# Kernel optimization log

Hardware: AMD Instinct MI355X
Metric: run time of the kernel (lower is better)

## Reference

```python
import jax, jax.numpy as jnp
import numpy as np

N, E, F_IN, C, ED = 10000, 40000, 128, 32, 4000
NEG_SLOPE = 0.2


def setup_inputs() -> dict:
    key = jax.random.key(0)
    ks = jax.random.split(key, 16)
    s = 0.05
    return {
        "x": jax.random.normal(ks[0], (N, F_IN), jnp.float32),
        "edge_index": jax.random.randint(ks[1], (2, E), 0, N, dtype=jnp.int64),
        "edge_attr": jax.random.normal(ks[2], (E, ED), jnp.float32),
        # layer 1 params
        "W1": jax.random.normal(ks[3], (F_IN, C), jnp.float32) * s,
        "a_src1": jax.random.normal(ks[4], (C,), jnp.float32) * s,
        "a_dst1": jax.random.normal(ks[5], (C,), jnp.float32) * s,
        "We1": jax.random.normal(ks[6], (ED, C), jnp.float32) * s,
        "a_e1": jax.random.normal(ks[7], (C,), jnp.float32) * s,
        "b1": jnp.zeros((C,), jnp.float32),
        # layer 2 params
        "W2": jax.random.normal(ks[8], (C, C), jnp.float32) * s,
        "a_src2": jax.random.normal(ks[9], (C,), jnp.float32) * s,
        "a_dst2": jax.random.normal(ks[10], (C,), jnp.float32) * s,
        "We2": jax.random.normal(ks[11], (ED, C), jnp.float32) * s,
        "a_e2": jax.random.normal(ks[12], (C,), jnp.float32) * s,
        "b2": jnp.zeros((C,), jnp.float32),
    }


def gat_layer(x, src, dst, edge_attr, W, a_src, a_dst, We, a_e, b):
    # node transform (shared src/dst linear, heads=1)
    h = x @ W                                   # [N, C]
    # project edge features first (lin_edge has no bias, so this commutes
    # with the 'mean' fill of self-loop edge_attr)
    e_proj = edge_attr @ We                     # [E, C]
    # self-loop edge features = scatter-mean of projected edge_attr by dst
    cnt = jax.ops.segment_sum(jnp.ones((src.shape[0],), h.dtype), dst, N)
    loop_e = jax.ops.segment_sum(e_proj, dst, N) / jnp.maximum(cnt, 1.0)[:, None]
    # append self loops -> E_full = E + N (static)
    ar = jnp.arange(N, dtype=src.dtype)
    src_f = jnp.concatenate([src, ar])
    dst_f = jnp.concatenate([dst, ar])
    e_full = jnp.concatenate([e_proj, loop_e], axis=0)   # [E+N, C]
    # attention logits
    alpha = (h @ a_src)[src_f] + (h @ a_dst)[dst_f] + e_full @ a_e
    alpha = jax.nn.leaky_relu(alpha, NEG_SLOPE)
    # segment softmax over incoming edges of each destination node
    m = jax.ops.segment_max(alpha, dst_f, N)
    alpha = jnp.exp(alpha - m[dst_f])
    denom = jax.ops.segment_sum(alpha, dst_f, N)
    alpha = alpha / (denom[dst_f] + 1e-16)
    # weighted scatter-add aggregation
    out = jax.ops.segment_sum(h[src_f] * alpha[:, None], dst_f, N)
    return out + b


def reference(x, edge_index, edge_attr,
              W1, a_src1, a_dst1, We1, a_e1, b1,
              W2, a_src2, a_dst2, We2, a_e2, b2):
    src, dst = edge_index[0], edge_index[1]
    z = gat_layer(x, src, dst, edge_attr, W1, a_src1, a_dst1, We1, a_e1, b1)
    z = jax.nn.relu(z)
    z = gat_layer(z, src, dst, edge_attr, W2, a_src2, a_dst2, We2, a_e2, b2)
    return z
```

## Files before the change

kernel.cpp:

```cpp
#include <hip/hip_runtime.h>

#define NN   10000
#define EE   40000
#define FIN  128
#define CC   32
#define EDIM 4000

#define OFF_CNT      0
#define OFF_EA1      10240
#define OFF_EA2      50240
#define OFF_SEA1     90240
#define OFF_SEA2     100480
#define OFF_DEN1     110720
#define OFF_DEN2     120960
#define OFF_AGG1     131200
#define OFF_AGG2     451200
#define ZERO_FLOATS  771200
#define OFF_SRC      771200
#define OFF_DST      812160
#define OFF_H1       853120
#define OFF_HS1      1173120
#define OFF_HD1      1183360
#define OFF_P1       1193600
#define OFF_PL1      1234560
#define OFF_Z1       1244800
#define OFF_H2       1564800
#define OFF_HS2      1884800
#define OFF_HD2      1895040
#define OFF_P2       1905280
#define OFF_PL2      1946240

__global__ __launch_bounds__(256) void detect_convert(
    const void* __restrict__ ei, int* __restrict__ srcI, int* __restrict__ dstI,
    int* __restrict__ cnt)
{
    const int* w = (const int*)ei;
    bool is64 = ((w[1] | w[3] | w[5] | w[7] | w[9] | w[11] | w[13] | w[15]) == 0);
    int i = blockIdx.x * 256 + threadIdx.x;
    if (i < EE) {
        int s, d;
        if (is64) {
            const long long* e64 = (const long long*)ei;
            s = (int)e64[i];
            d = (int)e64[EE + i];
        } else {
            s = w[i];
            d = w[EE + i];
        }
        srcI[i] = s;
        dstI[i] = d;
        atomicAdd(&cnt[d], 1);
    }
}

__global__ __launch_bounds__(256) void edge_gemm(
    const float* __restrict__ EA,
    const float* __restrict__ We1, const float* __restrict__ We2,
    const float* __restrict__ ae1, const float* __restrict__ ae2,
    float* __restrict__ ea1g, float* __restrict__ ea2g)
{
    __shared__ __align__(16) float As[64][68];
    __shared__ __align__(16) float Bs[64][68];

    const int t    = threadIdx.x;
    const int row0 = blockIdx.x * 64;
    const int c0   = blockIdx.y * 16;
    const int c1   = min(c0 + 16, 63);

    const int tm = t >> 4, tn = t & 15;
    const int lrow = t >> 2, ls = t & 3;

    float acc[4][4] = {};

    const float* Arow = EA + (size_t)(row0 + lrow) * EDIM;

    for (int ch = c0; ch < c1; ++ch) {
        const int k0 = ch * 64;
        #pragma unroll
        for (int j = 0; j < 4; ++j) {
            int kk = 4 * (ls + 4 * j);
            int kg = k0 + kk;
            float4 v = make_float4(0.f, 0.f, 0.f, 0.f);
            if (kg < EDIM) v = *(const float4*)(Arow + kg);
            As[kk + 0][lrow] = v.x;
            As[kk + 1][lrow] = v.y;
            As[kk + 2][lrow] = v.z;
            As[kk + 3][lrow] = v.w;
        }
        {
            int kg = k0 + lrow;
            #pragma unroll
            for (int j = 0; j < 4; ++j) {
                int col4 = 4 * (ls + 4 * j);
                float4 v = make_float4(0.f, 0.f, 0.f, 0.f);
                if (kg < EDIM) {
                    const float* src = (col4 < 32)
                        ? (We1 + (size_t)kg * 32 + col4)
                        : (We2 + (size_t)kg * 32 + (col4 - 32));
                    v = *(const float4*)src;
                }
                *(float4*)&Bs[lrow][col4] = v;
            }
        }
        __syncthreads();
        #pragma unroll 4
        for (int kk = 0; kk < 64; ++kk) {
            float4 a4 = *(float4*)&As[kk][tm << 2];
            float4 b4 = *(float4*)&Bs[kk][tn << 2];
            float av[4] = {a4.x, a4.y, a4.z, a4.w};
            float bv[4] = {b4.x, b4.y, b4.z, b4.w};
            #pragma unroll
            for (int i = 0; i < 4; ++i)
                #pragma unroll
                for (int j = 0; j < 4; ++j)
                    acc[i][j] += av[i] * bv[j];
        }
        __syncthreads();
    }

    float* red = &As[0][0];
    if (t < 128) red[t] = 0.f;
    __syncthreads();
    const int half = tn >> 3;
    const int colL = (tn << 2) - (half << 5);
    const float* ae = half ? ae2 : ae1;
    const float a0 = ae[colL], a1 = ae[colL + 1], a2 = ae[colL + 2], a3 = ae[colL + 3];
    #pragma unroll
    for (int i = 0; i < 4; ++i) {
        float sP = acc[i][0] * a0 + acc[i][1] * a1 + acc[i][2] * a2 + acc[i][3] * a3;
        atomicAdd(&red[(((tm << 2) + i) << 1) + half], sP);
    }
    __syncthreads();
    if (t < 128) {
        int row = t >> 1, hh = t & 1;
        float* dstp = hh ? ea2g : ea1g;
        atomicAdd(&dstp[row0 + row], red[t]);
    }
}

__global__ __launch_bounds__(256) void scatter_sum_ea(
    const int* __restrict__ dstI,
    const float* __restrict__ ea1, const float* __restrict__ ea2,
    float* __restrict__ se1, float* __restrict__ se2)
{
    int i = blockIdx.x * 256 + threadIdx.x;
    if (i < EE) {
        int d = dstI[i];
        atomicAdd(&se1[d], ea1[i]);
        atomicAdd(&se2[d], ea2[i]);
    }
}

template <int K>
__global__ __launch_bounds__(256) void node_transform(
    const float* __restrict__ X, const float* __restrict__ Wg,
    const float* __restrict__ a_src, const float* __restrict__ a_dst,
    float* __restrict__ h, float* __restrict__ hs, float* __restrict__ hd)
{
    __shared__ __align__(16) float Wl[K * 32];
    __shared__ __align__(16) float Xl[64][K];
    __shared__ float Hl[64][33];

    const int t = threadIdx.x;
    const int row0 = blockIdx.x * 64;

    for (int idx = t; idx < K * 8; idx += 256)
        ((float4*)Wl)[idx] = ((const float4*)Wg)[idx];
    for (int idx = t; idx < 64 * (K / 4); idx += 256) {
        int r = idx / (K / 4), kq = idx % (K / 4);
        int gr = row0 + r;
        float4 v = make_float4(0.f, 0.f, 0.f, 0.f);
        if (gr < NN) v = ((const float4*)(X + (size_t)gr * K))[kq];
        *(float4*)&Xl[r][kq * 4] = v;
    }
    __syncthreads();

    const int c = t & 31, rb = t >> 5;
    #pragma unroll
    for (int j = 0; j < 8; ++j) {
        int r = rb * 8 + j;
        float accv = 0.f;
        for (int k = 0; k < K; ++k) accv += Xl[r][k] * Wl[k * 32 + c];
        Hl[r][c] = accv;
        int gr = row0 + r;
        if (gr < NN) h[(size_t)gr * 32 + c] = accv;
    }
    __syncthreads();

    if (t < 64) {
        int gr = row0 + t;
        if (gr < NN) {
            float s1 = 0.f, s2 = 0.f;
            #pragma unroll
            for (int cc = 0; cc < 32; ++cc) {
                float hv = Hl[t][cc];
                s1 += hv * a_src[cc];
                s2 += hv * a_dst[cc];
            }
            hs[gr] = s1;
            hd[gr] = s2;
        }
    }
}

__global__ __launch_bounds__(256) void edge_softmax(
    const int* __restrict__ srcI, const int* __restrict__ dstI,
    const float* __restrict__ hs, const float* __restrict__ hd,
    const float* __restrict__ ea, const float* __restrict__ sum_ea,
    const int* __restrict__ cnt,
    float* __restrict__ pe, float* __restrict__ ploop, float* __restrict__ denom)
{
    int i = blockIdx.x * 256 + threadIdx.x;
    if (i < EE) {
        int s = srcI[i], d = dstI[i];
        float a = hs[s] + hd[d] + ea[i];
        a = a > 0.f ? a : 0.2f * a;
        float p = expf(a);
        pe[i] = p;
        atomicAdd(&denom[d], p);
    } else if (i < EE + NN) {
        int n = i - EE;
        float cf = (float)cnt[n];
        cf = cf < 1.f ? 1.f : cf;
        float a = hs[n] + hd[n] + sum_ea[n] / cf;
        a = a > 0.f ? a : 0.2f * a;
        float p = expf(a);
        ploop[n] = p;
        atomicAdd(&denom[n], p);
    }
}

__global__ __launch_bounds__(256) void aggregate(
    const int* __restrict__ srcI, const int* __restrict__ dstI,
    const float* __restrict__ h, const float* __restrict__ pe,
    const float* __restrict__ ploop, float* __restrict__ agg)
{
    int gid = blockIdx.x * 256 + threadIdx.x;
    int i = gid >> 3;
    int c4 = (gid & 7) << 2;
    if (i >= EE + NN) return;
    int s, d;
    float p;
    if (i < EE) {
        s = srcI[i]; d = dstI[i]; p = pe[i];
    } else {
        s = d = i - EE; p = ploop[s];
    }
    const float4 hv = *(const float4*)&h[(size_t)s * 32 + c4];
    float* ag = &agg[(size_t)d * 32 + c4];
    atomicAdd(ag + 0, p * hv.x);
    atomicAdd(ag + 1, p * hv.y);
    atomicAdd(ag + 2, p * hv.z);
    atomicAdd(ag + 3, p * hv.w);
}

__global__ __launch_bounds__(256) void finalize(
    const float* __restrict__ agg, const float* __restrict__ denom,
    const float* __restrict__ bias, float* __restrict__ out, int relu)
{
    int gid = blockIdx.x * 256 + threadIdx.x;
    if (gid >= NN * 32) return;
    int n = gid >> 5, cidx = gid & 31;
    float v = agg[gid] / (denom[n] + 1e-16f) + bias[cidx];
    if (relu) v = v > 0.f ? v : 0.f;
    out[gid] = v;
}

extern "C" void kernel_launch(void* const* d_in, const int* in_sizes, int n_in,
                              void* d_out, int out_size, void* d_ws, size_t ws_size,
                              hipStream_t stream)
{
    const float* x    = (const float*)d_in[0];
    const void*  ei   = d_in[1];
    const float* eatt = (const float*)d_in[2];
    const float* W1   = (const float*)d_in[3];
    const float* as1  = (const float*)d_in[4];
    const float* ad1  = (const float*)d_in[5];
    const float* We1  = (const float*)d_in[6];
    const float* ae1  = (const float*)d_in[7];
    const float* b1   = (const float*)d_in[8];
    const float* W2   = (const float*)d_in[9];
    const float* as2  = (const float*)d_in[10];
    const float* ad2  = (const float*)d_in[11];
    const float* We2  = (const float*)d_in[12];
    const float* ae2  = (const float*)d_in[13];
    const float* b2   = (const float*)d_in[14];
    float* out = (float*)d_out;
    float* w   = (float*)d_ws;

    hipMemsetAsync(d_ws, 0, (size_t)ZERO_FLOATS * 4, stream);

    int*   cnt  = (int*)(w + OFF_CNT);
    float* ea1v = w + OFF_EA1;
    float* ea2v = w + OFF_EA2;
    float* sea1 = w + OFF_SEA1;
    float* sea2 = w + OFF_SEA2;
    float* den1 = w + OFF_DEN1;
    float* den2 = w + OFF_DEN2;
    float* agg1 = w + OFF_AGG1;
    float* agg2 = w + OFF_AGG2;
    int*   srcI = (int*)(w + OFF_SRC);
    int*   dstI = (int*)(w + OFF_DST);
    float* h1   = w + OFF_H1;
    float* hs1  = w + OFF_HS1;
    float* hd1  = w + OFF_HD1;
    float* p1   = w + OFF_P1;
    float* pl1  = w + OFF_PL1;
    float* z1   = w + OFF_Z1;
    float* h2   = w + OFF_H2;
    float* hs2  = w + OFF_HS2;
    float* hd2  = w + OFF_HD2;
    float* p2   = w + OFF_P2;
    float* pl2  = w + OFF_PL2;

    detect_convert<<<157, 256, 0, stream>>>(ei, srcI, dstI, cnt);

    edge_gemm<<<dim3(625, 4), 256, 0, stream>>>(eatt, We1, We2, ae1, ae2, ea1v, ea2v);
    scatter_sum_ea<<<157, 256, 0, stream>>>(dstI, ea1v, ea2v, sea1, sea2);

    node_transform<128><<<157, 256, 0, stream>>>(x, W1, as1, ad1, h1, hs1, hd1);
    edge_softmax<<<196, 256, 0, stream>>>(srcI, dstI, hs1, hd1, ea1v, sea1, cnt, p1, pl1, den1);
    aggregate<<<1563, 256, 0, stream>>>(srcI, dstI, h1, p1, pl1, agg1);
    finalize<<<1250, 256, 0, stream>>>(agg1, den1, b1, z1, 1);

    node_transform<32><<<157, 256, 0, stream>>>(z1, W2, as2, ad2, h2, hs2, hd2);
    edge_softmax<<<196, 256, 0, stream>>>(srcI, dstI, hs2, hd2, ea2v, sea2, cnt, p2, pl2, den2);
    aggregate<<<1563, 256, 0, stream>>>(srcI, dstI, h2, p2, pl2, agg2);
    finalize<<<1250, 256, 0, stream>>>(agg2, den2, b2, out, 0);
}
```

Measured before the change: 1.094 ms.

## Reassociate edge projection into matvec and fuse softmax with aggregation

Precomputes We·a_e for both layers so the per-edge attention term becomes a dot product of each edge_attr row with a 4000-vector, replacing the tiled GEMM and separate scatter kernel; the scatter-sum of edge terms is folded into the same kernel. Edge softmax numerator and weighted aggregation are merged into a single kernel, dropping the stored per-edge probabilities. The node transform uses a transposed weight tile and vectorized inner loop. The cost becomes a streaming read of edge_attr; summation order changes slightly affect float rounding.

```diff
diff --git a/kernel.cpp b/kernel.cpp
--- a/kernel.cpp
+++ b/kernel.cpp
@@ -7,28 +7,26 @@
 #define EDIM 4000
 
 #define OFF_CNT      0
-#define OFF_EA1      10240
-#define OFF_EA2      50240
-#define OFF_SEA1     90240
-#define OFF_SEA2     100480
-#define OFF_DEN1     110720
-#define OFF_DEN2     120960
-#define OFF_AGG1     131200
-#define OFF_AGG2     451200
-#define ZERO_FLOATS  771200
-#define OFF_SRC      771200
-#define OFF_DST      812160
-#define OFF_H1       853120
-#define OFF_HS1      1173120
-#define OFF_HD1      1183360
-#define OFF_P1       1193600
-#define OFF_PL1      1234560
-#define OFF_Z1       1244800
-#define OFF_H2       1564800
-#define OFF_HS2      1884800
-#define OFF_HD2      1895040
-#define OFF_P2       1905280
-#define OFF_PL2      1946240
+#define OFF_SEA1     10240
+#define OFF_SEA2     20480
+#define OFF_DEN1     30720
+#define OFF_DEN2     40960
+#define OFF_AGG1     51200
+#define OFF_AGG2     371200
+#define ZERO_FLOATS  691200
+#define OFF_SRC      691200
+#define OFF_DST      732160
+#define OFF_EA1      773120
+#define OFF_EA2      814080
+#define OFF_W1V      855040
+#define OFF_W2V      859136
+#define OFF_H1       863232
+#define OFF_HS1      1183232
+#define OFF_HD1      1193472
+#define OFF_Z1       1203712
+#define OFF_H2       1523712
+#define OFF_HS2      1843712
+#define OFF_HD2      1853952
 
 __global__ __launch_bounds__(256) void detect_convert(
     const void* __restrict__ ei, int* __restrict__ srcI, int* __restrict__ dstI,
@@ -53,101 +51,86 @@
     }
 }
 
-__global__ __launch_bounds__(256) void edge_gemm(
+__global__ __launch_bounds__(256) void weight_vec(
+    const float* __restrict__ We1, const float* __restrict__ ae1,
+    const float* __restrict__ We2, const float* __restrict__ ae2,
+    float* __restrict__ w1, float* __restrict__ w2)
+{
+    __shared__ float a1s[32], a2s[32];
+    if (threadIdx.x < 32) {
+        a1s[threadIdx.x] = ae1[threadIdx.x];
+        a2s[threadIdx.x] = ae2[threadIdx.x];
+    }
+    __syncthreads();
+    int k = blockIdx.x * 256 + threadIdx.x;
+    if (k >= EDIM) return;
+    const float* r1 = We1 + (size_t)k * 32;
+    const float* r2 = We2 + (size_t)k * 32;
+    float s1 = 0.f, s2 = 0.f;
+    #pragma unroll
+    for (int c4 = 0; c4 < 8; ++c4) {
+        float4 v1 = ((const float4*)r1)[c4];
+        float4 v2 = ((const float4*)r2)[c4];
+        float4 a1 = *(const float4*)&a1s[c4 * 4];
+        float4 a2 = *(const float4*)&a2s[c4 * 4];
+        s1 += v1.x * a1.x + v1.y * a1.y + v1.z * a1.z + v1.w * a1.w;
+        s2 += v2.x * a2.x + v2.y * a2.y + v2.z * a2.z + v2.w * a2.w;
+    }
+    w1[k] = s1;
+    w2[k] = s2;
+}
+
+__global__ __launch_bounds__(256) void edge_dot(
     const float* __restrict__ EA,
-    const float* __restrict__ We1, const float* __restrict__ We2,
-    const float* __restrict__ ae1, const float* __restrict__ ae2,
-    float* __restrict__ ea1g, float* __restrict__ ea2g)
-{
-    __shared__ __align__(16) float As[64][68];
-    __shared__ __align__(16) float Bs[64][68];
-
-    const int t    = threadIdx.x;
-    const int row0 = blockIdx.x * 64;
-    const int c0   = blockIdx.y * 16;
-    const int c1   = min(c0 + 16, 63);
-
-    const int tm = t >> 4, tn = t & 15;
-    const int lrow = t >> 2, ls = t & 3;
-
-    float acc[4][4] = {};
-
-    const float* Arow = EA + (size_t)(row0 + lrow) * EDIM;
-
-    for (int ch = c0; ch < c1; ++ch) {
-        const int k0 = ch * 64;
+    const float* __restrict__ w1, const float* __restrict__ w2,
+    const int* __restrict__ dstI,
+    float* __restrict__ ea1, float* __restrict__ ea2,
+    float* __restrict__ sea1, float* __restrict__ sea2)
+{
+    __shared__ __align__(16) float W1s[4000];
+    __shared__ __align__(16) float W2s[4000];
+    const int t = threadIdx.x;
+    for (int i = t; i < 1000; i += 256) {
+        ((float4*)W1s)[i] = ((const float4*)w1)[i];
+        ((float4*)W2s)[i] = ((const float4*)w2)[i];
+    }
+    __syncthreads();
+    const int wv = t >> 6, l = t & 63;
+    const int base = blockIdx.x * 16;
+    #pragma unroll
+    for (int ee = 0; ee < 4; ++ee) {
+        const int e = base + ee * 4 + wv;
+        const float* A = EA + (size_t)e * EDIM;
+        float acc1 = 0.f, acc2 = 0.f;
+        #pragma unroll 5
+        for (int j = 0; j < 15; ++j) {
+            int idx = j * 256 + l * 4;
+            float4 a = *(const float4*)(A + idx);
+            float4 u = *(const float4*)(W1s + idx);
+            float4 v = *(const float4*)(W2s + idx);
+            acc1 += a.x * u.x + a.y * u.y + a.z * u.z + a.w * u.w;
+            acc2 += a.x * v.x + a.y * v.y + a.z * v.z + a.w * v.w;
+        }
+        if (l < 40) {
+            int idx = 3840 + l * 4;
+            float4 a = *(const float4*)(A + idx);
+            float4 u = *(const float4*)(W1s + idx);
+            float4 v = *(const float4*)(W2s + idx);
+            acc1 += a.x * u.x + a.y * u.y + a.z * u.z + a.w * u.w;
+            acc2 += a.x * v.x + a.y * v.y + a.z * v.z + a.w * v.w;
+        }
         #pragma unroll
-        for (int j = 0; j < 4; ++j) {
-            int kk = 4 * (ls + 4 * j);
-            int kg = k0 + kk;
-            float4 v = make_float4(0.f, 0.f, 0.f, 0.f);
-            if (kg < EDIM) v = *(const float4*)(Arow + kg);
-            As[kk + 0][lrow] = v.x;
-            As[kk + 1][lrow] = v.y;
-            As[kk + 2][lrow] = v.z;
-            As[kk + 3][lrow] = v.w;
-        }
-        {
-            int kg = k0 + lrow;
-            #pragma unroll
-            for (int j = 0; j < 4; ++j) {
-                int col4 = 4 * (ls + 4 * j);
-                float4 v = make_float4(0.f, 0.f, 0.f, 0.f);
-                if (kg < EDIM) {
-                    const float* src = (col4 < 32)
-                        ? (We1 + (size_t)kg * 32 + col4)
-                        : (We2 + (size_t)kg * 32 + (col4 - 32));
-                    v = *(const float4*)src;
-                }
-                *(float4*)&Bs[lrow][col4] = v;
-            }
-        }
-        __syncthreads();
-        #pragma unroll 4
-        for (int kk = 0; kk < 64; ++kk) {
-            float4 a4 = *(float4*)&As[kk][tm << 2];
-            float4 b4 = *(float4*)&Bs[kk][tn << 2];
-            float av[4] = {a4.x, a4.y, a4.z, a4.w};
-            float bv[4] = {b4.x, b4.y, b4.z, b4.w};
-            #pragma unroll
-            for (int i = 0; i < 4; ++i)
-                #pragma unroll
-                for (int j = 0; j < 4; ++j)
-                    acc[i][j] += av[i] * bv[j];
-        }
-        __syncthreads();
-    }
-
-    float* red = &As[0][0];
-    if (t < 128) red[t] = 0.f;
-    __syncthreads();
-    const int half = tn >> 3;
-    const int colL = (tn << 2) - (half << 5);
-    const float* ae = half ? ae2 : ae1;
-    const float a0 = ae[colL], a1 = ae[colL + 1], a2 = ae[colL + 2], a3 = ae[colL + 3];
-    #pragma unroll
-    for (int i = 0; i < 4; ++i) {
-        float sP = acc[i][0] * a0 + acc[i][1] * a1 + acc[i][2] * a2 + acc[i][3] * a3;
-        atomicAdd(&red[(((tm << 2) + i) << 1) + half], sP);
-    }
-    __syncthreads();
-    if (t < 128) {
-        int row = t >> 1, hh = t & 1;
-        float* dstp = hh ? ea2g : ea1g;
-        atomicAdd(&dstp[row0 + row], red[t]);
-    }
-}
-
-__global__ __launch_bounds__(256) void scatter_sum_ea(
-    const int* __restrict__ dstI,
-    const float* __restrict__ ea1, const float* __restrict__ ea2,
-    float* __restrict__ se1, float* __restrict__ se2)
-{
-    int i = blockIdx.x * 256 + threadIdx.x;
-    if (i < EE) {
-        int d = dstI[i];
-        atomicAdd(&se1[d], ea1[i]);
-        atomicAdd(&se2[d], ea2[i]);
+        for (int m = 32; m >= 1; m >>= 1) {
+            acc1 += __shfl_xor(acc1, m);
+            acc2 += __shfl_xor(acc2, m);
+        }
+        if (l == 0) {
+            ea1[e] = acc1;
+            ea2[e] = acc2;
+            int d = dstI[e];
+            atomicAdd(&sea1[d], acc1);
+            atomicAdd(&sea2[d], acc2);
+        }
     }
 }
 
@@ -157,15 +140,18 @@
     const float* __restrict__ a_src, const float* __restrict__ a_dst,
     float* __restrict__ h, float* __restrict__ hs, float* __restrict__ hd)
 {
-    __shared__ __align__(16) float Wl[K * 32];
+    constexpr int SW = K + 4;
+    __shared__ __align__(16) float Wt[32][SW];
     __shared__ __align__(16) float Xl[64][K];
     __shared__ float Hl[64][33];
 
     const int t = threadIdx.x;
     const int row0 = blockIdx.x * 64;
 
-    for (int idx = t; idx < K * 8; idx += 256)
-        ((float4*)Wl)[idx] = ((const float4*)Wg)[idx];
+    for (int idx = t; idx < 32 * K; idx += 256) {
+        int c = idx & 31, k = idx >> 5;
+        Wt[c][k] = Wg[idx];
+    }
     for (int idx = t; idx < 64 * (K / 4); idx += 256) {
         int r = idx / (K / 4), kq = idx % (K / 4);
         int gr = row0 + r;
@@ -176,14 +162,21 @@
     __syncthreads();
 
     const int c = t & 31, rb = t >> 5;
+    float acc[8] = {};
+    #pragma unroll 4
+    for (int k4 = 0; k4 < K / 4; ++k4) {
+        float4 wv = *(const float4*)&Wt[c][k4 * 4];
+        #pragma unroll
+        for (int j = 0; j < 8; ++j) {
+            float4 xv = *(const float4*)&Xl[rb * 8 + j][k4 * 4];
+            acc[j] += xv.x * wv.x + xv.y * wv.y + xv.z * wv.z + xv.w * wv.w;
+        }
+    }
     #pragma unroll
     for (int j = 0; j < 8; ++j) {
-        int r = rb * 8 + j;
-        float accv = 0.f;
-        for (int k = 0; k < K; ++k) accv += Xl[r][k] * Wl[k * 32 + c];
-        Hl[r][c] = accv;
-        int gr = row0 + r;
-        if (gr < NN) h[(size_t)gr * 32 + c] = accv;
+        int r = rb * 8 + j, gr = row0 + r;
+        Hl[r][c] = acc[j];
+        if (gr < NN) h[(size_t)gr * 32 + c] = acc[j];
     }
     __syncthreads();
 
@@ -203,51 +196,33 @@
     }
 }
 
-__global__ __launch_bounds__(256) void edge_softmax(
+__global__ __launch_bounds__(256) void attn_agg(
     const int* __restrict__ srcI, const int* __restrict__ dstI,
     const float* __restrict__ hs, const float* __restrict__ hd,
-    const float* __restrict__ ea, const float* __restrict__ sum_ea,
-    const int* __restrict__ cnt,
-    float* __restrict__ pe, float* __restrict__ ploop, float* __restrict__ denom)
-{
-    int i = blockIdx.x * 256 + threadIdx.x;
-    if (i < EE) {
-        int s = srcI[i], d = dstI[i];
-        float a = hs[s] + hd[d] + ea[i];
-        a = a > 0.f ? a : 0.2f * a;
-        float p = expf(a);
-        pe[i] = p;
-        atomicAdd(&denom[d], p);
-    } else if (i < EE + NN) {
-        int n = i - EE;
-        float cf = (float)cnt[n];
-        cf = cf < 1.f ? 1.f : cf;
-        float a = hs[n] + hd[n] + sum_ea[n] / cf;
-        a = a > 0.f ? a : 0.2f * a;
-        float p = expf(a);
-        ploop[n] = p;
-        atomicAdd(&denom[n], p);
-    }
-}
-
-__global__ __launch_bounds__(256) void aggregate(
-    const int* __restrict__ srcI, const int* __restrict__ dstI,
-    const float* __restrict__ h, const float* __restrict__ pe,
-    const float* __restrict__ ploop, float* __restrict__ agg)
+    const float* __restrict__ ea, const float* __restrict__ sea,
+    const int* __restrict__ cnt, const float* __restrict__ h,
+    float* __restrict__ denom, float* __restrict__ agg)
 {
     int gid = blockIdx.x * 256 + threadIdx.x;
-    int i = gid >> 3;
-    int c4 = (gid & 7) << 2;
+    int i = gid >> 3, sub = gid & 7;
     if (i >= EE + NN) return;
     int s, d;
-    float p;
+    float extra;
     if (i < EE) {
-        s = srcI[i]; d = dstI[i]; p = pe[i];
+        s = srcI[i];
+        d = dstI[i];
+        extra = ea[i];
     } else {
-        s = d = i - EE; p = ploop[s];
-    }
-    const float4 hv = *(const float4*)&h[(size_t)s * 32 + c4];
-    float* ag = &agg[(size_t)d * 32 + c4];
+        s = d = i - EE;
+        float cf = (float)cnt[s];
+        extra = sea[s] / (cf < 1.f ? 1.f : cf);
+    }
+    float a = hs[s] + hd[d] + extra;
+    a = a > 0.f ? a : 0.2f * a;
+    float p = expf(a);
+    if (sub == 0) atomicAdd(&denom[d], p);
+    const float4 hv = *(const float4*)&h[(size_t)s * 32 + sub * 4];
+    float* ag = &agg[(size_t)d * 32 + sub * 4];
     atomicAdd(ag + 0, p * hv.x);
     atomicAdd(ag + 1, p * hv.y);
     atomicAdd(ag + 2, p * hv.z);
@@ -291,8 +266,6 @@
     hipMemsetAsync(d_ws, 0, (size_t)ZERO_FLOATS * 4, stream);
 
     int*   cnt  = (int*)(w + OFF_CNT);
-    float* ea1v = w + OFF_EA1;
-    float* ea2v = w + OFF_EA2;
     float* sea1 = w + OFF_SEA1;
     float* sea2 = w + OFF_SEA2;
     float* den1 = w + OFF_DEN1;
@@ -301,30 +274,28 @@
     float* agg2 = w + OFF_AGG2;
     int*   srcI = (int*)(w + OFF_SRC);
     int*   dstI = (int*)(w + OFF_DST);
+    float* ea1v = w + OFF_EA1;
+    float* ea2v = w + OFF_EA2;
+    float* w1v  = w + OFF_W1V;
+    float* w2v  = w + OFF_W2V;
     float* h1   = w + OFF_H1;
     float* hs1  = w + OFF_HS1;
     float* hd1  = w + OFF_HD1;
-    float* p1   = w + OFF_P1;
-    float* pl1  = w + OFF_PL1;
     float* z1   = w + OFF_Z1;
     float* h2   = w + OFF_H2;
     float* hs2  = w + OFF_HS2;
     float* hd2  = w + OFF_HD2;
-    float* p2   = w + OFF_P2;
-    float* pl2  = w + OFF_PL2;
 
     detect_convert<<<157, 256, 0, stream>>>(ei, srcI, dstI, cnt);
-
-    edge_gemm<<<dim3(625, 4), 256, 0, stream>>>(eatt, We1, We2, ae1, ae2, ea1v, ea2v);
-    scatter_sum_ea<<<157, 256, 0, stream>>>(dstI, ea1v, ea2v, sea1, sea2);
+    weight_vec<<<16, 256, 0, stream>>>(We1, ae1, We2, ae2, w1v, w2v);
+
+    edge_dot<<<2500, 256, 0, stream>>>(eatt, w1v, w2v, dstI, ea1v, ea2v, sea1, sea2);
 
     node_transform<128><<<157, 256, 0, stream>>>(x, W1, as1, ad1, h1, hs1, hd1);
-    edge_softmax<<<196, 256, 0, stream>>>(srcI, dstI, hs1, hd1, ea1v, sea1, cnt, p1, pl1, den1);
-    aggregate<<<1563, 256, 0, stream>>>(srcI, dstI, h1, p1, pl1, agg1);
+    attn_agg<<<1563, 256, 0, stream>>>(srcI, dstI, hs1, hd1, ea1v, sea1, cnt, h1, den1, agg1);
     finalize<<<1250, 256, 0, stream>>>(agg1, den1, b1, z1, 1);
 
     node_transform<32><<<157, 256, 0, stream>>>(z1, W2, as2, ad2, h2, hs2, hd2);
-    edge_softmax<<<196, 256, 0, stream>>>(srcI, dstI, hs2, hd2, ea2v, sea2, cnt, p2, pl2, den2);
-    aggregate<<<1563, 256, 0, stream>>>(srcI, dstI, h2, p2, pl2, agg2);
+    attn_agg<<<1563, 256, 0, stream>>>(srcI, dstI, hs2, hd2, ea2v, sea2, cnt, h2, den2, agg2);
     finalize<<<1250, 256, 0, stream>>>(agg2, den2, b2, out, 0);
 }
```

After: 916.7 us. 16.2% less time.
